# Kernel optimization log

Hardware: AMD Instinct MI355X
Metric: run time of the kernel (lower is better)

Reference implementation:

```python
import jax, jax.numpy as jnp
import numpy as np

N = 50000      # nodes
E = 600000     # edges
H = 128        # hidden_features (= in_features)
ED = 16        # edge_attr_dim
B = 256        # number of graphs in batch
L = 5          # num_layers
OUT = 128      # out_features


def _xavier(key, shape):
    fan_in, fan_out = shape
    a = float(np.sqrt(6.0 / (fan_in + fan_out)))
    return jax.random.uniform(key, shape, jnp.float32, -a, a)


def setup_inputs() -> dict:
    key = jax.random.key(0)
    ks = jax.random.split(key, 32)
    x = jax.random.normal(ks[0], (N, H), jnp.float32)
    edge_index = jax.random.randint(ks[1], (2, E), 0, N, jnp.int32)
    edge_attr = jax.random.normal(ks[2], (E, ED), jnp.float32)
    batch = jnp.sort(jax.random.randint(ks[3], (N,), 0, B, jnp.int32))
    # per-layer parameters, stacked along leading L axis (in=hidden so uniform)
    node_W = jnp.stack([_xavier(jax.random.fold_in(ks[4], i), (H, H)) for i in range(L)])
    edge_W = jnp.stack([_xavier(jax.random.fold_in(ks[5], i), (ED, H)) for i in range(L)])
    mlp1_W = jnp.stack([_xavier(jax.random.fold_in(ks[6], i), (H, H)) for i in range(L)])
    mlp2_W = jnp.stack([_xavier(jax.random.fold_in(ks[7], i), (H, H)) for i in range(L)])
    zb = jnp.zeros((L, H), jnp.float32)
    # virtual-node update MLP (shared across layers) and final classifier
    vn_w0 = _xavier(ks[8], (H, H)); vn_b0 = jnp.zeros((H,), jnp.float32)
    vn_w1 = _xavier(ks[9], (H, H)); vn_b1 = jnp.zeros((H,), jnp.float32)
    fc_W = _xavier(ks[10], (H, OUT)); fc_b = jnp.zeros((OUT,), jnp.float32)
    vn_init = jnp.zeros((1, H), jnp.float32)  # embedding initialized to 0
    return {
        "x": x, "edge_attr": edge_attr,
        "node_W": node_W, "node_b": zb, "edge_W": edge_W, "edge_b": zb,
        "mlp1_W": mlp1_W, "mlp1_b": zb, "mlp2_W": mlp2_W, "mlp2_b": zb,
        "vn_w0": vn_w0, "vn_b0": vn_b0, "vn_w1": vn_w1, "vn_b1": vn_b1,
        "fc_W": fc_W, "fc_b": fc_b, "vn_init": vn_init,
        "edge_index": edge_index, "batch": batch,
    }


def reference(x, edge_attr, node_W, node_b, edge_W, edge_b, mlp1_W, mlp1_b,
              mlp2_W, mlp2_b, vn_w0, vn_b0, vn_w1, vn_b1, fc_W, fc_b,
              vn_init, edge_index, batch):
    src, dst = edge_index[0], edge_index[1]
    # per-graph node counts for mean pooling (guard against empty graphs)
    counts = jnp.maximum(
        jax.ops.segment_sum(jnp.ones((N, 1), x.dtype), batch, num_segments=B), 1.0)
    vn = jnp.broadcast_to(vn_init, (B, H))  # weight.repeat(batch_size, 1)

    def layer(carry, p):
        xc, vn = carry
        nW, nb, eW, eb, m1W, m1b, m2W, m2b = p
        h = xc @ nW + nb + vn[batch]              # node encode + VN broadcast
        ea = edge_attr @ eW + eb                   # edge encode [E,H]
        msg = h[src] + ea                          # gather + add
        agg = jax.ops.segment_sum(msg, dst, num_segments=N)  # scatter-add
        out = jax.nn.relu(agg @ m1W + m1b) @ m2W + m2b        # layer MLP
        xn = jax.nn.relu(out)
        pooled = jax.ops.segment_sum(xn, batch, num_segments=B) / counts
        vn2 = vn + jax.nn.relu(jax.nn.relu(pooled @ vn_w0 + vn_b0) @ vn_w1 + vn_b1)
        return (xn, vn2), None

    (xf, _), _ = jax.lax.scan(
        layer, (x, vn),
        (node_W, node_b, edge_W, edge_b, mlp1_W, mlp1_b, mlp2_W, mlp2_b))
    pooled = jax.ops.segment_sum(xf, batch, num_segments=B) / counts
    return pooled @ fc_W + fc_b
```

## Files before the change

kernel.cpp:

```cpp
#include <hip/hip_runtime.h>

#define NN 50000
#define EE 600000
#define HH 128
#define EDD 16
#define BB 256
#define LL 5
#define NN16 (NN * 16)
#define NSHADOW 8
#define GN 782

typedef float f32x4 __attribute__((ext_vector_type(4)));
typedef _Float16 f16x4 __attribute__((ext_vector_type(4)));
typedef _Float16 f16x8 __attribute__((ext_vector_type(8)));

__global__ __launch_bounds__(256) void wprep_all_k(
    const float* __restrict__ W0, const float* __restrict__ W1, const float* __restrict__ W2,
    _Float16* __restrict__ H0, _Float16* __restrict__ L0,
    _Float16* __restrict__ H1, _Float16* __restrict__ L1,
    _Float16* __restrict__ H2, _Float16* __restrict__ L2,
    const float* __restrict__ eW, const float* __restrict__ eb, const float* __restrict__ nb,
    _Float16* __restrict__ BXh, _Float16* __restrict__ BXl)
{
    int idx = blockIdx.x * 256 + threadIdx.x;
    if (idx < 3 * 81920) {
        int seg = idx / 81920, r = idx - seg * 81920;
        const float* W = (seg == 0) ? W0 : (seg == 1) ? W1 : W2;
        _Float16* Wh = (seg == 0) ? H0 : (seg == 1) ? H1 : H2;
        _Float16* Wl = (seg == 0) ? L0 : (seg == 1) ? L1 : L2;
        int mat = r >> 14;
        int rr = r & 16383;
        int j = rr & 7, lane = (rr >> 3) & 63, ks = (rr >> 9) & 3, ntw = (rr >> 11) & 7;
        int lm = lane & 15, quad = lane >> 4;
        int n = (ntw >> 1) * 32 + (ntw & 1) * 16 + lm;
        int k = ks * 32 + quad * 8 + j;
        float w = W[(mat << 14) + (k << 7) + n];
        _Float16 h = (_Float16)w;
        Wh[r] = h;
        Wl[r] = (_Float16)(w - (float)h);
    } else {
        int i2 = idx - 3 * 81920;
        if (i2 >= 5 * 8192) return;
        int j = i2 & 7, lane = (i2 >> 3) & 63, ks = (i2 >> 9) & 1, ntw = (i2 >> 10) & 7, l = i2 >> 13;
        int lm = lane & 15, quad = lane >> 4;
        int n = (ntw >> 1) * 32 + (ntw & 1) * 16 + lm;
        int k = ks * 32 + quad * 8 + j;
        float v = 0.f;
        if (k < 16) v = eW[((size_t)l * 16 + k) * 128 + n];
        else if (k < 32) v = eW[((size_t)l * 16 + (k - 16)) * 128 + n];
        else if (k == 32) v = eb[l * 128 + n] + nb[l * 128 + n];
        _Float16 h = (_Float16)v;
        BXh[i2] = h;
        BXl[i2] = (_Float16)(v - (float)h);
    }
}

__global__ __launch_bounds__(256) void misc_k(const float* __restrict__ x, _Float16* __restrict__ X0,
    const float* __restrict__ vninit, float* __restrict__ vn, _Float16* __restrict__ vnB,
    float* __restrict__ pooled8)
{
    int i = blockIdx.x * 256 + threadIdx.x;
    if (i < NN * 32) {
        float4 v = ((const float4*)x)[i];
        f16x4 o;
        o[0] = (_Float16)v.x; o[1] = (_Float16)v.y; o[2] = (_Float16)v.z; o[3] = (_Float16)v.w;
        ((f16x4*)X0)[i] = o;
    } else {
        int k = i - NN * 32;
        if (k < NSHADOW * BB * HH) pooled8[k] = 0.f;
        if (k < BB * HH) { vn[k] = vninit[k & 127]; vnB[k] = (_Float16)0; }
    }
}

__device__ __forceinline__ void mfma_stage16(
    const _Float16* __restrict__ As,
    const _Float16* __restrict__ Wh, const _Float16* __restrict__ Wl,
    int wn, int lm, int quad, int lane, f32x4 acc[4][2])
{
    f16x8 Bh[2][4], Bl[2][4];
#pragma unroll
    for (int nt = 0; nt < 2; ++nt)
#pragma unroll
        for (int ks = 0; ks < 4; ++ks) {
            int fi = ((((wn * 2 + nt) * 4) + ks) * 64 + lane) * 8;
            Bh[nt][ks] = *(const f16x8*)(Wh + fi);
            Bl[nt][ks] = *(const f16x8*)(Wl + fi);
        }
#pragma unroll
    for (int ks = 0; ks < 4; ++ks) {
        f16x8 a[4];
#pragma unroll
        for (int mt = 0; mt < 4; ++mt) {
            int off = (mt * 16 + lm) * 136 + ks * 32 + quad * 8;
            a[mt] = *(const f16x8*)(As + off);
        }
#pragma unroll
        for (int mt = 0; mt < 4; ++mt)
#pragma unroll
            for (int nt = 0; nt < 2; ++nt) {
                acc[mt][nt] = __builtin_amdgcn_mfma_f32_16x16x32_f16(a[mt], Bh[nt][ks], acc[mt][nt], 0, 0, 0);
                acc[mt][nt] = __builtin_amdgcn_mfma_f32_16x16x32_f16(a[mt], Bl[nt][ks], acc[mt][nt], 0, 0, 0);
            }
    }
}

__device__ __forceinline__ void store_f16(const _Float16* __restrict__ Fo,
    _Float16* __restrict__ out, int M, int brow, int tid)
{
    const int r = tid >> 2, cg = tid & 3;
    const int grow = brow + r;
    if (grow >= M) return;
    const f16x8* src = (const f16x8*)(Fo + r * 136 + cg * 32);
    f16x8* dst = (f16x8*)(out + (size_t)grow * 128 + cg * 32);
#pragma unroll
    for (int i = 0; i < 4; ++i) dst[i] = src[i];
}

__global__ __launch_bounds__(256) void layer_k(
    const _Float16* __restrict__ Xin,
    const _Float16* __restrict__ Afix,
    const _Float16* __restrict__ Cfrag, const _Float16* __restrict__ vnB, int usevn,
    const int* __restrict__ rowstart, const int2* __restrict__ csr,
    const _Float16* __restrict__ WNh, const _Float16* __restrict__ WNl,
    const _Float16* __restrict__ BXh, const _Float16* __restrict__ BXl,
    const _Float16* __restrict__ W1h, const _Float16* __restrict__ W1l, const float* __restrict__ b1,
    const _Float16* __restrict__ W2h, const _Float16* __restrict__ W2l, const float* __restrict__ b2,
    _Float16* __restrict__ Xout, float* __restrict__ pooled8,
    const int* __restrict__ batch, int M)
{
    __shared__ __align__(16) _Float16 bufA[64 * 136];
    __shared__ __align__(16) _Float16 bufB[64 * 136];
    const int tid = threadIdx.x, brow = blockIdx.x * 64;

    {
        const int r = tid >> 2, cg = tid & 3;
        const int grow = brow + r;
        _Float16* p = bufB + r * 72 + cg * 16;
        if (grow < M) {
            const f16x8* s = (const f16x8*)(Afix + (size_t)grow * 64 + cg * 16);
            ((f16x8*)p)[0] = s[0]; ((f16x8*)p)[1] = s[1];
        } else {
            f16x8 z = (f16x8)(_Float16)0;
            ((f16x8*)p)[0] = z; ((f16x8*)p)[1] = z;
        }
    }

    {
        const int wv = tid >> 6, grp = (tid >> 4) & 3, li = tid & 15;
        const f16x8* X8 = (const f16x8*)Xin;
        for (int j = 0; j < 4; ++j) {
            int rnode = wv * 16 + grp * 4 + j;
            int node = brow + rnode;
            f16x8 o = (f16x8)(_Float16)0;
            if (node < M) {
                int s = rowstart[node], e = rowstart[node + 1];
                float ax[8];
#pragma unroll
                for (int k = 0; k < 8; ++k) ax[k] = 0.f;
                int p = s;
                for (; p + 4 <= e; p += 4) {
                    int s0 = csr[p].x, s1 = csr[p + 1].x, s2 = csr[p + 2].x, s3 = csr[p + 3].x;
                    f16x8 x0 = X8[(size_t)s0 * 16 + li];
                    f16x8 x1 = X8[(size_t)s1 * 16 + li];
                    f16x8 x2 = X8[(size_t)s2 * 16 + li];
                    f16x8 x3 = X8[(size_t)s3 * 16 + li];
#pragma unroll
                    for (int k = 0; k < 8; ++k)
                        ax[k] += ((float)x0[k] + (float)x1[k]) + ((float)x2[k] + (float)x3[k]);
                }
                for (; p < e; ++p) {
                    f16x8 x0 = X8[(size_t)csr[p].x * 16 + li];
#pragma unroll
                    for (int k = 0; k < 8; ++k) ax[k] += (float)x0[k];
                }
#pragma unroll
                for (int k = 0; k < 8; ++k) o[k] = (_Float16)ax[k];
            }
            *(f16x8*)(bufA + rnode * 136 + li * 8) = o;
        }
    }
    __syncthreads();

    const int lane = tid & 63, wn = tid >> 6, lm = lane & 15, quad = lane >> 4;
    const int colb = wn * 32 + lm;

    f32x4 acc[4][2];
#pragma unroll
    for (int mt = 0; mt < 4; ++mt) { acc[mt][0] = (f32x4)(0.f); acc[mt][1] = (f32x4)(0.f); }

    mfma_stage16(bufA, WNh, WNl, wn, lm, quad, lane, acc);

#pragma unroll
    for (int ksf = 0; ksf < 2; ++ksf) {
        f16x8 Bh[2], Bl[2];
#pragma unroll
        for (int nt = 0; nt < 2; ++nt) {
            int fi = (((wn * 2 + nt) * 2 + ksf) * 64 + lane) * 8;
            Bh[nt] = *(const f16x8*)(BXh + fi);
            Bl[nt] = *(const f16x8*)(BXl + fi);
        }
#pragma unroll
        for (int mt = 0; mt < 4; ++mt) {
            f16x8 a = *(const f16x8*)(bufB + (mt * 16 + lm) * 72 + ksf * 32 + quad * 8);
#pragma unroll
            for (int nt = 0; nt < 2; ++nt) {
                acc[mt][nt] = __builtin_amdgcn_mfma_f32_16x16x32_f16(a, Bh[nt], acc[mt][nt], 0, 0, 0);
                acc[mt][nt] = __builtin_amdgcn_mfma_f32_16x16x32_f16(a, Bl[nt], acc[mt][nt], 0, 0, 0);
            }
        }
    }

    if (usevn) {
        const _Float16* Cb = Cfrag + (size_t)blockIdx.x * 16384;
#pragma unroll
        for (int ks = 0; ks < 8; ++ks) {
            f16x8 bv[2];
#pragma unroll
            for (int nt = 0; nt < 2; ++nt)
                bv[nt] = *(const f16x8*)(vnB + (((ks * 8 + (wn * 2 + nt)) * 64 + lane) * 8));
#pragma unroll
            for (int mt = 0; mt < 4; ++mt) {
                f16x8 av = *(const f16x8*)(Cb + (((mt * 8 + ks) * 64 + lane) * 8));
                acc[mt][0] = __builtin_amdgcn_mfma_f32_16x16x32_f16(av, bv[0], acc[mt][0], 0, 0, 0);
                acc[mt][1] = __builtin_amdgcn_mfma_f32_16x16x32_f16(av, bv[1], acc[mt][1], 0, 0, 0);
            }
        }
    }
    __syncthreads();

#pragma unroll
    for (int mt = 0; mt < 4; ++mt) {
#pragma unroll
        for (int r = 0; r < 4; ++r) {
            int trow = mt * 16 + quad * 4 + r;
            bufA[trow * 136 + colb]      = (_Float16)acc[mt][0][r];
            bufA[trow * 136 + colb + 16] = (_Float16)acc[mt][1][r];
        }
    }
    __syncthreads();

#pragma unroll
    for (int mt = 0; mt < 4; ++mt) { acc[mt][0] = (f32x4)(0.f); acc[mt][1] = (f32x4)(0.f); }
    mfma_stage16(bufA, W1h, W1l, wn, lm, quad, lane, acc);
    {
        const float c0 = b1[colb], c1 = b1[colb + 16];
#pragma unroll
        for (int mt = 0; mt < 4; ++mt) {
#pragma unroll
            for (int r = 0; r < 4; ++r) {
                int trow = mt * 16 + quad * 4 + r;
                bufB[trow * 136 + colb]      = (_Float16)fmaxf(acc[mt][0][r] + c0, 0.f);
                bufB[trow * 136 + colb + 16] = (_Float16)fmaxf(acc[mt][1][r] + c1, 0.f);
            }
        }
    }
    __syncthreads();

#pragma unroll
    for (int mt = 0; mt < 4; ++mt) { acc[mt][0] = (f32x4)(0.f); acc[mt][1] = (f32x4)(0.f); }
    mfma_stage16(bufB, W2h, W2l, wn, lm, quad, lane, acc);
    {
        const float d0 = b2[colb], d1 = b2[colb + 16];
#pragma unroll
        for (int mt = 0; mt < 4; ++mt) {
#pragma unroll
            for (int r = 0; r < 4; ++r) {
                int trow = mt * 16 + quad * 4 + r;
                bufA[trow * 136 + colb]      = (_Float16)fmaxf(acc[mt][0][r] + d0, 0.f);
                bufA[trow * 136 + colb + 16] = (_Float16)fmaxf(acc[mt][1][r] + d1, 0.f);
            }
        }
    }
    __syncthreads();
    store_f16(bufA, Xout, M, brow, tid);

    {
        float* pooled = pooled8 + (size_t)(blockIdx.x & (NSHADOW - 1)) * (BB * HH);
        const int c = tid & 127, half = tid >> 7;
        const int row0 = half * 32;
        float sum = 0.f;
        int curg = -1;
        for (int r2 = 0; r2 < 32; ++r2) {
            int grow = brow + row0 + r2;
            if (grow >= M) break;
            int g = batch[grow];
            if (g != curg) {
                if (curg >= 0) atomicAdd(&pooled[curg * 128 + c], sum);
                curg = g; sum = 0.f;
            }
            sum += (float)bufA[(row0 + r2) * 136 + c];
        }
        if (curg >= 0) atomicAdd(&pooled[curg * 128 + c], sum);
    }
}

__global__ __launch_bounds__(256) void aggfix_k(
    const float* __restrict__ eattr, const int* __restrict__ rowstart,
    const int2* __restrict__ csr, _Float16* __restrict__ Afix, int n)
{
    const int lane = threadIdx.x & 15;
    const int node = blockIdx.x * 16 + (threadIdx.x >> 4);
    if (node >= n) return;
    const int s = rowstart[node], e = rowstart[node + 1];
    float acc = 0.f;
    for (int p = s; p < e; ++p)
        acc += eattr[(size_t)csr[p].y * 16 + lane];
    _Float16 hi = (_Float16)acc;
    _Float16 lo = (_Float16)(acc - (float)hi);
    _Float16* A = Afix + (size_t)node * 64;
    A[lane] = hi;
    A[16 + lane] = lo;
    A[32 + lane] = (lane == 0) ? (_Float16)(float)(e - s) : (_Float16)0;
    A[48 + lane] = (_Float16)0;
}

__global__ void histboth_k(const int* __restrict__ dstv, const int* __restrict__ srcv,
                           const int* __restrict__ batch,
                           int* __restrict__ degp, unsigned int* __restrict__ Cpack)
{
    int i = blockIdx.x * 256 + threadIdx.x;
    if (i >= EE) return;
    int d = dstv[i];
    atomicAdd(&degp[(blockIdx.x & 3) * NN16 + (d << 4)], 1);
    int g = batch[srcv[i]];
    int blk = d >> 6, rib = d & 63, mt = rib >> 4, lm = rib & 15;
    int ks = g >> 5, quad = (g >> 3) & 3, j = g & 7;
    size_t e = (size_t)blk * 16384 + (size_t)(((mt * 8 + ks) * 64) + quad * 16 + lm) * 8 + j;
    atomicAdd(&Cpack[e >> 1], 1u << ((e & 1) * 16));
}

__global__ __launch_bounds__(256) void ccvt_k(unsigned int* __restrict__ Cpack)
{
    int i = blockIdx.x * 256 + threadIdx.x;
    if (i >= GN * 16384 / 2) return;
    unsigned int v = Cpack[i];
    _Float16 lo = (_Float16)(float)(v & 0xffffu);
    _Float16 hi = (_Float16)(float)(v >> 16);
    unsigned short lu = __builtin_bit_cast(unsigned short, lo);
    unsigned short hu = __builtin_bit_cast(unsigned short, hi);
    Cpack[i] = (unsigned int)lu | ((unsigned int)hu << 16);
}

__global__ __launch_bounds__(128) void vn_update_k(
    float* __restrict__ pooled8, const int* __restrict__ gstart,
    const float* __restrict__ W0, const float* __restrict__ b0,
    const float* __restrict__ W1, const float* __restrict__ b1,
    float* __restrict__ vn, _Float16* __restrict__ vnB)
{
    __shared__ float p[128], q[128];
    const int g = blockIdx.x, t = threadIdx.x;
    float cnt = (float)(gstart[g + 1] - gstart[g]);
    if (cnt < 1.f) cnt = 1.f;
    float sum = 0.f;
#pragma unroll
    for (int s = 0; s < NSHADOW; ++s) {
        float* slot = pooled8 + (size_t)s * (BB * HH) + g * 128 + t;
        sum += *slot;
        *slot = 0.f;
    }
    p[t] = sum / cnt;
    __syncthreads();
    float a0 = b0[t];
    for (int k = 0; k < 128; ++k) a0 = fmaf(p[k], W0[k * 128 + t], a0);
    q[t] = fmaxf(a0, 0.f);
    __syncthreads();
    float a1 = b1[t];
    for (int k = 0; k < 128; ++k) a1 = fmaf(q[k], W1[k * 128 + t], a1);
    float nv = vn[g * 128 + t] + fmaxf(a1, 0.f);
    vn[g * 128 + t] = nv;
    {
        int ks = g >> 5, quad = (g >> 3) & 3, j = g & 7;
        int tt = ((t >> 5) << 1) | ((t >> 4) & 1);
        int lanev = quad * 16 + (t & 15);
        vnB[((ks * 8 + tt) * 64 + lanev) * 8 + j] = (_Float16)nv;
    }
}

__global__ __launch_bounds__(128) void fc_k(
    const float* __restrict__ pooled8, const int* __restrict__ gstart,
    const float* __restrict__ W, const float* __restrict__ b,
    float* __restrict__ out)
{
    __shared__ float p[128];
    const int g = blockIdx.x, t = threadIdx.x;
    float cnt = (float)(gstart[g + 1] - gstart[g]);
    if (cnt < 1.f) cnt = 1.f;
    float sum = 0.f;
#pragma unroll
    for (int s = 0; s < NSHADOW; ++s)
        sum += pooled8[(size_t)s * (BB * HH) + g * 128 + t];
    p[t] = sum / cnt;
    __syncthreads();
    float acc = b[t];
    for (int k = 0; k < 128; ++k) acc = fmaf(p[k], W[k * 128 + t], acc);
    out[g * 128 + t] = acc;
}

__global__ void scan_deg_k(const int* __restrict__ degp, int n, int* __restrict__ out, int* __restrict__ bsum)
{
    __shared__ int s[256];
    int gid = blockIdx.x * 256 + threadIdx.x;
    int v = 0;
    if (gid < n) {
        int o = gid << 4;
        v = degp[o] + degp[NN16 + o] + degp[2 * NN16 + o] + degp[3 * NN16 + o];
    }
    s[threadIdx.x] = v;
    __syncthreads();
    for (int off = 1; off < 256; off <<= 1) {
        int t = (threadIdx.x >= off) ? s[threadIdx.x - off] : 0;
        __syncthreads();
        s[threadIdx.x] += t;
        __syncthreads();
    }
    int incl = s[threadIdx.x];
    if (gid < n) out[gid] = incl - v;
    if (bsum != nullptr && threadIdx.x == 255) bsum[blockIdx.x] = incl;
}

__global__ void scan_k(const int* __restrict__ in, int n, int* __restrict__ out,
                       const int* __restrict__ batch, int* __restrict__ gstart)
{
    __shared__ int s[256];
    int v = (threadIdx.x < n) ? in[threadIdx.x] : 0;
    s[threadIdx.x] = v;
    __syncthreads();
    for (int off = 1; off < 256; off <<= 1) {
        int t = (threadIdx.x >= off) ? s[threadIdx.x - off] : 0;
        __syncthreads();
        s[threadIdx.x] += t;
        __syncthreads();
    }
    if (threadIdx.x < n) out[threadIdx.x] = s[threadIdx.x] - v;
    {
        int b = threadIdx.x;
        int lo = 0, hi = NN;
        while (lo < hi) {
            int mid = (lo + hi) >> 1;
            if (batch[mid] < b) lo = mid + 1; else hi = mid;
        }
        gstart[b] = lo;
        if (threadIdx.x == 0) gstart[BB] = NN;
    }
}

__global__ void addoff_k(int* __restrict__ data, const int* __restrict__ boff,
                         int* __restrict__ cursorp, int n, int total)
{
    int i = blockIdx.x * 256 + threadIdx.x;
    if (i < n) {
        int v = data[i] + boff[blockIdx.x];
        data[i] = v;
        cursorp[i << 4] = v;
    }
    if (i == 0) data[n] = total;
}

__global__ void fill_k(const int* __restrict__ dst, const int* __restrict__ src, int n,
                       int* __restrict__ cursorp, int2* __restrict__ csr)
{
    int e = blockIdx.x * 256 + threadIdx.x;
    if (e < n) {
        int slot = atomicAdd(&cursorp[dst[e] << 4], 1);
        int2 pr; pr.x = src[e]; pr.y = e;
        csr[slot] = pr;
    }
}

extern "C" void kernel_launch(void* const* d_in, const int* in_sizes, int n_in,
                              void* d_out, int out_size, void* d_ws, size_t ws_size,
                              hipStream_t stream)
{
    (void)in_sizes; (void)n_in; (void)out_size; (void)ws_size;
    const float* x       = (const float*)d_in[0];
    const float* eattr   = (const float*)d_in[1];
    const float* node_W  = (const float*)d_in[2];
    const float* node_b  = (const float*)d_in[3];
    const float* edge_W  = (const float*)d_in[4];
    const float* edge_b  = (const float*)d_in[5];
    const float* mlp1_W  = (const float*)d_in[6];
    const float* mlp1_b  = (const float*)d_in[7];
    const float* mlp2_W  = (const float*)d_in[8];
    const float* mlp2_b  = (const float*)d_in[9];
    const float* vn_w0   = (const float*)d_in[10];
    const float* vn_b0   = (const float*)d_in[11];
    const float* vn_w1   = (const float*)d_in[12];
    const float* vn_b1   = (const float*)d_in[13];
    const float* fc_W    = (const float*)d_in[14];
    const float* fc_b    = (const float*)d_in[15];
    const float* vn_init = (const float*)d_in[16];
    const int*   eidx    = (const int*)d_in[17];
    const int*   batch   = (const int*)d_in[18];
    const int* srcv = eidx;
    const int* dstv = eidx + EE;

    char* wp = (char*)d_ws;
    auto alloc = [&](size_t bytes) -> void* {
        void* p = (void*)wp;
        wp += (bytes + 255) & ~(size_t)255;
        return p;
    };
    int* degp       = (int*)alloc((size_t)4 * NN16 * 4);
    _Float16* Cfrag = (_Float16*)alloc((size_t)GN * 16384 * 2);
    const size_t zero_bytes = (size_t)4 * NN16 * 4 + (size_t)GN * 16384 * 2;

    _Float16* X0   = (_Float16*)alloc((size_t)NN * HH * 2);
    _Float16* X1   = (_Float16*)alloc((size_t)NN * HH * 2);
    _Float16* X2   = (_Float16*)alloc((size_t)NN * HH * 2);
    _Float16* Afix = (_Float16*)alloc((size_t)NN * 64 * 2);
    float* vn      = (float*)alloc((size_t)BB * HH * 4);
    _Float16* vnB  = (_Float16*)alloc((size_t)BB * HH * 2);
    float* pooled8 = (float*)alloc((size_t)NSHADOW * BB * HH * 4);
    int* rowstart  = (int*)alloc((size_t)(NN + 1) * 4);
    int* cursorp   = (int*)alloc((size_t)NN16 * 4);
    int2* csr      = (int2*)alloc((size_t)EE * 8);
    int* bsum      = (int*)alloc(256 * 4);
    int* boff      = (int*)alloc(256 * 4);
    int* gstart    = (int*)alloc((size_t)(BB + 1) * 4);
    _Float16* WtN_h = (_Float16*)alloc((size_t)5 * 16384 * 2);
    _Float16* WtN_l = (_Float16*)alloc((size_t)5 * 16384 * 2);
    _Float16* Wt1_h = (_Float16*)alloc((size_t)5 * 16384 * 2);
    _Float16* Wt1_l = (_Float16*)alloc((size_t)5 * 16384 * 2);
    _Float16* Wt2_h = (_Float16*)alloc((size_t)5 * 16384 * 2);
    _Float16* Wt2_l = (_Float16*)alloc((size_t)5 * 16384 * 2);
    _Float16* BXh   = (_Float16*)alloc((size_t)5 * 8192 * 2);
    _Float16* BXl   = (_Float16*)alloc((size_t)5 * 8192 * 2);

    (void)hipMemsetAsync(degp, 0, zero_bytes, stream);

    histboth_k<<<(EE + 255) / 256, 256, 0, stream>>>(dstv, srcv, batch, degp, (unsigned int*)Cfrag);

    const int NB1 = (NN + 255) / 256;
    scan_deg_k<<<NB1, 256, 0, stream>>>(degp, NN, rowstart, bsum);
    scan_k<<<1, 256, 0, stream>>>(bsum, NB1, boff, batch, gstart);
    addoff_k<<<NB1, 256, 0, stream>>>(rowstart, boff, cursorp, NN, EE);
    fill_k<<<(EE + 255) / 256, 256, 0, stream>>>(dstv, srcv, EE, cursorp, csr);
    aggfix_k<<<(NN + 15) / 16, 256, 0, stream>>>(eattr, rowstart, csr, Afix, NN);
    ccvt_k<<<(GN * 16384 / 2 + 255) / 256, 256, 0, stream>>>((unsigned int*)Cfrag);

    misc_k<<<(NN * 32 + NSHADOW * BB * HH) / 256, 256, 0, stream>>>(x, X0, vn_init, vn, vnB, pooled8);
    wprep_all_k<<<(3 * 81920 + 5 * 8192) / 256, 256, 0, stream>>>(
        node_W, mlp1_W, mlp2_W, WtN_h, WtN_l, Wt1_h, Wt1_l, Wt2_h, Wt2_l,
        edge_W, edge_b, node_b, BXh, BXl);

    const _Float16* xin = X0;
    for (int l = 0; l < LL; ++l) {
        _Float16* xout = (l & 1) ? X2 : X1;
        layer_k<<<GN, 256, 0, stream>>>(xin, Afix, Cfrag, vnB, (l > 0) ? 1 : 0,
            rowstart, csr,
            WtN_h + (size_t)l * 16384, WtN_l + (size_t)l * 16384,
            BXh + (size_t)l * 8192, BXl + (size_t)l * 8192,
            Wt1_h + (size_t)l * 16384, Wt1_l + (size_t)l * 16384, mlp1_b + (size_t)l * HH,
            Wt2_h + (size_t)l * 16384, Wt2_l + (size_t)l * 16384, mlp2_b + (size_t)l * HH,
            xout, pooled8, batch, NN);
        if (l < LL - 1)
            vn_update_k<<<BB, 128, 0, stream>>>(pooled8, gstart, vn_w0, vn_b0, vn_w1, vn_b1, vn, vnB);
        xin = xout;
    }
    fc_k<<<BB, 128, 0, stream>>>(pooled8, gstart, fc_W, fc_b, (float*)d_out);
}
```

Baseline: 558.6 us.

## Split layer kernel work across 8 waves with 16-column MFMA tiles

```diff
diff --git a/kernel.cpp b/kernel.cpp
--- a/kernel.cpp
+++ b/kernel.cpp
@@ -72,20 +72,18 @@
     }
 }
 
-__device__ __forceinline__ void mfma_stage16(
+__device__ __forceinline__ void mfma_stage8w(
     const _Float16* __restrict__ As,
     const _Float16* __restrict__ Wh, const _Float16* __restrict__ Wl,
-    int wn, int lm, int quad, int lane, f32x4 acc[4][2])
-{
-    f16x8 Bh[2][4], Bl[2][4];
-#pragma unroll
-    for (int nt = 0; nt < 2; ++nt)
-#pragma unroll
-        for (int ks = 0; ks < 4; ++ks) {
-            int fi = ((((wn * 2 + nt) * 4) + ks) * 64 + lane) * 8;
-            Bh[nt][ks] = *(const f16x8*)(Wh + fi);
-            Bl[nt][ks] = *(const f16x8*)(Wl + fi);
-        }
+    int wn, int lm, int quad, int lane, f32x4 acc[4])
+{
+    f16x8 Bh[4], Bl[4];
+#pragma unroll
+    for (int ks = 0; ks < 4; ++ks) {
+        int fi = ((wn * 4 + ks) * 64 + lane) * 8;
+        Bh[ks] = *(const f16x8*)(Wh + fi);
+        Bl[ks] = *(const f16x8*)(Wl + fi);
+    }
 #pragma unroll
     for (int ks = 0; ks < 4; ++ks) {
         f16x8 a[4];
@@ -95,28 +93,14 @@
             a[mt] = *(const f16x8*)(As + off);
         }
 #pragma unroll
-        for (int mt = 0; mt < 4; ++mt)
-#pragma unroll
-            for (int nt = 0; nt < 2; ++nt) {
-                acc[mt][nt] = __builtin_amdgcn_mfma_f32_16x16x32_f16(a[mt], Bh[nt][ks], acc[mt][nt], 0, 0, 0);
-                acc[mt][nt] = __builtin_amdgcn_mfma_f32_16x16x32_f16(a[mt], Bl[nt][ks], acc[mt][nt], 0, 0, 0);
-            }
-    }
-}
-
-__device__ __forceinline__ void store_f16(const _Float16* __restrict__ Fo,
-    _Float16* __restrict__ out, int M, int brow, int tid)
-{
-    const int r = tid >> 2, cg = tid & 3;
-    const int grow = brow + r;
-    if (grow >= M) return;
-    const f16x8* src = (const f16x8*)(Fo + r * 136 + cg * 32);
-    f16x8* dst = (f16x8*)(out + (size_t)grow * 128 + cg * 32);
-#pragma unroll
-    for (int i = 0; i < 4; ++i) dst[i] = src[i];
-}
-
-__global__ __launch_bounds__(256) void layer_k(
+        for (int mt = 0; mt < 4; ++mt) {
+            acc[mt] = __builtin_amdgcn_mfma_f32_16x16x32_f16(a[mt], Bh[ks], acc[mt], 0, 0, 0);
+            acc[mt] = __builtin_amdgcn_mfma_f32_16x16x32_f16(a[mt], Bl[ks], acc[mt], 0, 0, 0);
+        }
+    }
+}
+
+__global__ __launch_bounds__(512, 6) void layer_k(
     const _Float16* __restrict__ Xin,
     const _Float16* __restrict__ Afix,
     const _Float16* __restrict__ Cfrag, const _Float16* __restrict__ vnB, int usevn,
@@ -133,23 +117,22 @@
     const int tid = threadIdx.x, brow = blockIdx.x * 64;
 
     {
-        const int r = tid >> 2, cg = tid & 3;
+        const int r = tid >> 3, cg = tid & 7;
         const int grow = brow + r;
-        _Float16* p = bufB + r * 72 + cg * 16;
+        _Float16* p = bufB + r * 72 + cg * 8;
         if (grow < M) {
-            const f16x8* s = (const f16x8*)(Afix + (size_t)grow * 64 + cg * 16);
-            ((f16x8*)p)[0] = s[0]; ((f16x8*)p)[1] = s[1];
+            *(f16x8*)p = *(const f16x8*)(Afix + (size_t)grow * 64 + cg * 8);
         } else {
-            f16x8 z = (f16x8)(_Float16)0;
-            ((f16x8*)p)[0] = z; ((f16x8*)p)[1] = z;
-        }
-    }
-
-    {
-        const int wv = tid >> 6, grp = (tid >> 4) & 3, li = tid & 15;
+            *(f16x8*)p = (f16x8)(_Float16)0;
+        }
+    }
+
+    {
+        const int gid = tid >> 4, li = tid & 15;
         const f16x8* X8 = (const f16x8*)Xin;
-        for (int j = 0; j < 4; ++j) {
-            int rnode = wv * 16 + grp * 4 + j;
+#pragma unroll
+        for (int j = 0; j < 2; ++j) {
+            int rnode = gid * 2 + j;
             int node = brow + rnode;
             f16x8 o = (f16x8)(_Float16)0;
             if (node < M) {
@@ -182,31 +165,22 @@
     __syncthreads();
 
     const int lane = tid & 63, wn = tid >> 6, lm = lane & 15, quad = lane >> 4;
-    const int colb = wn * 32 + lm;
-
-    f32x4 acc[4][2];
-#pragma unroll
-    for (int mt = 0; mt < 4; ++mt) { acc[mt][0] = (f32x4)(0.f); acc[mt][1] = (f32x4)(0.f); }
-
-    mfma_stage16(bufA, WNh, WNl, wn, lm, quad, lane, acc);
+    const int colb = (wn >> 1) * 32 + (wn & 1) * 16 + lm;
+
+    f32x4 acc[4];
+#pragma unroll
+    for (int mt = 0; mt < 4; ++mt) acc[mt] = (f32x4)(0.f);
 
 #pragma unroll
     for (int ksf = 0; ksf < 2; ++ksf) {
-        f16x8 Bh[2], Bl[2];
-#pragma unroll
-        for (int nt = 0; nt < 2; ++nt) {
-            int fi = (((wn * 2 + nt) * 2 + ksf) * 64 + lane) * 8;
-            Bh[nt] = *(const f16x8*)(BXh + fi);
-            Bl[nt] = *(const f16x8*)(BXl + fi);
-        }
+        int fi = ((wn * 2 + ksf) * 64 + lane) * 8;
+        f16x8 Bh = *(const f16x8*)(BXh + fi);
+        f16x8 Bl = *(const f16x8*)(BXl + fi);
 #pragma unroll
         for (int mt = 0; mt < 4; ++mt) {
             f16x8 a = *(const f16x8*)(bufB + (mt * 16 + lm) * 72 + ksf * 32 + quad * 8);
-#pragma unroll
-            for (int nt = 0; nt < 2; ++nt) {
-                acc[mt][nt] = __builtin_amdgcn_mfma_f32_16x16x32_f16(a, Bh[nt], acc[mt][nt], 0, 0, 0);
-                acc[mt][nt] = __builtin_amdgcn_mfma_f32_16x16x32_f16(a, Bl[nt], acc[mt][nt], 0, 0, 0);
-            }
+            acc[mt] = __builtin_amdgcn_mfma_f32_16x16x32_f16(a, Bh, acc[mt], 0, 0, 0);
+            acc[mt] = __builtin_amdgcn_mfma_f32_16x16x32_f16(a, Bl, acc[mt], 0, 0, 0);
         }
     }
 
@@ -214,18 +188,16 @@
         const _Float16* Cb = Cfrag + (size_t)blockIdx.x * 16384;
 #pragma unroll
         for (int ks = 0; ks < 8; ++ks) {
-            f16x8 bv[2];
-#pragma unroll
-            for (int nt = 0; nt < 2; ++nt)
-                bv[nt] = *(const f16x8*)(vnB + (((ks * 8 + (wn * 2 + nt)) * 64 + lane) * 8));
+            f16x8 bv = *(const f16x8*)(vnB + (((ks * 8 + wn) * 64 + lane) * 8));
 #pragma unroll
             for (int mt = 0; mt < 4; ++mt) {
                 f16x8 av = *(const f16x8*)(Cb + (((mt * 8 + ks) * 64 + lane) * 8));
-                acc[mt][0] = __builtin_amdgcn_mfma_f32_16x16x32_f16(av, bv[0], acc[mt][0], 0, 0, 0);
-                acc[mt][1] = __builtin_amdgcn_mfma_f32_16x16x32_f16(av, bv[1], acc[mt][1], 0, 0, 0);
+                acc[mt] = __builtin_amdgcn_mfma_f32_16x16x32_f16(av, bv, acc[mt], 0, 0, 0);
             }
         }
     }
+
+    mfma_stage8w(bufA, WNh, WNl, wn, lm, quad, lane, acc);
     __syncthreads();
 
 #pragma unroll
@@ -233,54 +205,61 @@
 #pragma unroll
         for (int r = 0; r < 4; ++r) {
             int trow = mt * 16 + quad * 4 + r;
-            bufA[trow * 136 + colb]      = (_Float16)acc[mt][0][r];
-            bufA[trow * 136 + colb + 16] = (_Float16)acc[mt][1][r];
-        }
-    }
-    __syncthreads();
-
-#pragma unroll
-    for (int mt = 0; mt < 4; ++mt) { acc[mt][0] = (f32x4)(0.f); acc[mt][1] = (f32x4)(0.f); }
-    mfma_stage16(bufA, W1h, W1l, wn, lm, quad, lane, acc);
-    {
-        const float c0 = b1[colb], c1 = b1[colb + 16];
+            bufA[trow * 136 + colb] = (_Float16)acc[mt][r];
+        }
+    }
+    __syncthreads();
+
+#pragma unroll
+    for (int mt = 0; mt < 4; ++mt) acc[mt] = (f32x4)(0.f);
+    mfma_stage8w(bufA, W1h, W1l, wn, lm, quad, lane, acc);
+    {
+        const float c0 = b1[colb];
 #pragma unroll
         for (int mt = 0; mt < 4; ++mt) {
 #pragma unroll
             for (int r = 0; r < 4; ++r) {
                 int trow = mt * 16 + quad * 4 + r;
-                bufB[trow * 136 + colb]      = (_Float16)fmaxf(acc[mt][0][r] + c0, 0.f);
-                bufB[trow * 136 + colb + 16] = (_Float16)fmaxf(acc[mt][1][r] + c1, 0.f);
+                bufB[trow * 136 + colb] = (_Float16)fmaxf(acc[mt][r] + c0, 0.f);
             }
         }
     }
     __syncthreads();
 
 #pragma unroll
-    for (int mt = 0; mt < 4; ++mt) { acc[mt][0] = (f32x4)(0.f); acc[mt][1] = (f32x4)(0.f); }
-    mfma_stage16(bufB, W2h, W2l, wn, lm, quad, lane, acc);
-    {
-        const float d0 = b2[colb], d1 = b2[colb + 16];
+    for (int mt = 0; mt < 4; ++mt) acc[mt] = (f32x4)(0.f);
+    mfma_stage8w(bufB, W2h, W2l, wn, lm, quad, lane, acc);
+    {
+        const float d0 = b2[colb];
 #pragma unroll
         for (int mt = 0; mt < 4; ++mt) {
 #pragma unroll
             for (int r = 0; r < 4; ++r) {
                 int trow = mt * 16 + quad * 4 + r;
-                bufA[trow * 136 + colb]      = (_Float16)fmaxf(acc[mt][0][r] + d0, 0.f);
-                bufA[trow * 136 + colb + 16] = (_Float16)fmaxf(acc[mt][1][r] + d1, 0.f);
+                bufA[trow * 136 + colb] = (_Float16)fmaxf(acc[mt][r] + d0, 0.f);
             }
         }
     }
     __syncthreads();
-    store_f16(bufA, Xout, M, brow, tid);
+
+    {
+        const int r = tid >> 3, cg = tid & 7;
+        const int grow = brow + r;
+        if (grow < M) {
+            const f16x8* src = (const f16x8*)(bufA + r * 136 + cg * 16);
+            f16x8* dst = (f16x8*)(Xout + (size_t)grow * 128 + cg * 16);
+            dst[0] = src[0];
+            dst[1] = src[1];
+        }
+    }
 
     {
         float* pooled = pooled8 + (size_t)(blockIdx.x & (NSHADOW - 1)) * (BB * HH);
-        const int c = tid & 127, half = tid >> 7;
-        const int row0 = half * 32;
+        const int c = tid & 127, seg = tid >> 7;
+        const int row0 = seg * 16;
         float sum = 0.f;
         int curg = -1;
-        for (int r2 = 0; r2 < 32; ++r2) {
+        for (int r2 = 0; r2 < 16; ++r2) {
             int grow = brow + row0 + r2;
             if (grow >= M) break;
             int g = batch[grow];
@@ -546,7 +525,7 @@
     const _Float16* xin = X0;
     for (int l = 0; l < LL; ++l) {
         _Float16* xout = (l & 1) ? X2 : X1;
-        layer_k<<<GN, 256, 0, stream>>>(xin, Afix, Cfrag, vnB, (l > 0) ? 1 : 0,
+        layer_k<<<GN, 512, 0, stream>>>(xin, Afix, Cfrag, vnB, (l > 0) ? 1 : 0,
             rowstart, csr,
             WtN_h + (size_t)l * 16384, WtN_l + (size_t)l * 16384,
             BXh + (size_t)l * 8192, BXl + (size_t)l * 8192,
```

New measurement: 588.9 us. 1.05x slower.

## Halve layer kernel row tile to 32 rows and double grid

Applied to the files above, without the earlier changes.

```diff
diff --git a/kernel.cpp b/kernel.cpp
--- a/kernel.cpp
+++ b/kernel.cpp
@@ -9,6 +9,7 @@
 #define NN16 (NN * 16)
 #define NSHADOW 8
 #define GN 782
+#define GN2 1563
 
 typedef float f32x4 __attribute__((ext_vector_type(4)));
 typedef _Float16 f16x4 __attribute__((ext_vector_type(4)));
@@ -72,10 +73,10 @@
     }
 }
 
-__device__ __forceinline__ void mfma_stage16(
+__device__ __forceinline__ void mfma_stage32(
     const _Float16* __restrict__ As,
     const _Float16* __restrict__ Wh, const _Float16* __restrict__ Wl,
-    int wn, int lm, int quad, int lane, f32x4 acc[4][2])
+    int wn, int lm, int quad, int lane, f32x4 acc[2][2])
 {
     f16x8 Bh[2][4], Bl[2][4];
 #pragma unroll
@@ -88,32 +89,20 @@
         }
 #pragma unroll
     for (int ks = 0; ks < 4; ++ks) {
-        f16x8 a[4];
-#pragma unroll
-        for (int mt = 0; mt < 4; ++mt) {
+        f16x8 a[2];
+#pragma unroll
+        for (int mt = 0; mt < 2; ++mt) {
             int off = (mt * 16 + lm) * 136 + ks * 32 + quad * 8;
             a[mt] = *(const f16x8*)(As + off);
         }
 #pragma unroll
-        for (int mt = 0; mt < 4; ++mt)
+        for (int mt = 0; mt < 2; ++mt)
 #pragma unroll
             for (int nt = 0; nt < 2; ++nt) {
                 acc[mt][nt] = __builtin_amdgcn_mfma_f32_16x16x32_f16(a[mt], Bh[nt][ks], acc[mt][nt], 0, 0, 0);
                 acc[mt][nt] = __builtin_amdgcn_mfma_f32_16x16x32_f16(a[mt], Bl[nt][ks], acc[mt][nt], 0, 0, 0);
             }
     }
-}
-
-__device__ __forceinline__ void store_f16(const _Float16* __restrict__ Fo,
-    _Float16* __restrict__ out, int M, int brow, int tid)
-{
-    const int r = tid >> 2, cg = tid & 3;
-    const int grow = brow + r;
-    if (grow >= M) return;
-    const f16x8* src = (const f16x8*)(Fo + r * 136 + cg * 32);
-    f16x8* dst = (f16x8*)(out + (size_t)grow * 128 + cg * 32);
-#pragma unroll
-    for (int i = 0; i < 4; ++i) dst[i] = src[i];
 }
 
 __global__ __launch_bounds__(256) void layer_k(
@@ -128,28 +117,27 @@
     _Float16* __restrict__ Xout, float* __restrict__ pooled8,
     const int* __restrict__ batch, int M)
 {
-    __shared__ __align__(16) _Float16 bufA[64 * 136];
-    __shared__ __align__(16) _Float16 bufB[64 * 136];
-    const int tid = threadIdx.x, brow = blockIdx.x * 64;
-
-    {
-        const int r = tid >> 2, cg = tid & 3;
+    __shared__ __align__(16) _Float16 bufA[32 * 136];
+    __shared__ __align__(16) _Float16 bufB[32 * 136];
+    const int tid = threadIdx.x, brow = blockIdx.x * 32;
+
+    {
+        const int r = tid >> 3, cg = tid & 7;
         const int grow = brow + r;
-        _Float16* p = bufB + r * 72 + cg * 16;
+        _Float16* p = bufB + r * 72 + cg * 8;
         if (grow < M) {
-            const f16x8* s = (const f16x8*)(Afix + (size_t)grow * 64 + cg * 16);
-            ((f16x8*)p)[0] = s[0]; ((f16x8*)p)[1] = s[1];
+            *(f16x8*)p = *(const f16x8*)(Afix + (size_t)grow * 64 + cg * 8);
         } else {
-            f16x8 z = (f16x8)(_Float16)0;
-            ((f16x8*)p)[0] = z; ((f16x8*)p)[1] = z;
-        }
-    }
-
-    {
-        const int wv = tid >> 6, grp = (tid >> 4) & 3, li = tid & 15;
+            *(f16x8*)p = (f16x8)(_Float16)0;
+        }
+    }
+
+    {
+        const int gid = tid >> 4, li = tid & 15;
         const f16x8* X8 = (const f16x8*)Xin;
-        for (int j = 0; j < 4; ++j) {
-            int rnode = wv * 16 + grp * 4 + j;
+#pragma unroll
+        for (int j = 0; j < 2; ++j) {
+            int rnode = gid * 2 + j;
             int node = brow + rnode;
             f16x8 o = (f16x8)(_Float16)0;
             if (node < M) {
@@ -184,11 +172,9 @@
     const int lane = tid & 63, wn = tid >> 6, lm = lane & 15, quad = lane >> 4;
     const int colb = wn * 32 + lm;
 
-    f32x4 acc[4][2];
-#pragma unroll
-    for (int mt = 0; mt < 4; ++mt) { acc[mt][0] = (f32x4)(0.f); acc[mt][1] = (f32x4)(0.f); }
-
-    mfma_stage16(bufA, WNh, WNl, wn, lm, quad, lane, acc);
+    f32x4 acc[2][2];
+#pragma unroll
+    for (int mt = 0; mt < 2; ++mt) { acc[mt][0] = (f32x4)(0.f); acc[mt][1] = (f32x4)(0.f); }
 
 #pragma unroll
     for (int ksf = 0; ksf < 2; ++ksf) {
@@ -200,7 +186,7 @@
             Bl[nt] = *(const f16x8*)(BXl + fi);
         }
 #pragma unroll
-        for (int mt = 0; mt < 4; ++mt) {
+        for (int mt = 0; mt < 2; ++mt) {
             f16x8 a = *(const f16x8*)(bufB + (mt * 16 + lm) * 72 + ksf * 32 + quad * 8);
 #pragma unroll
             for (int nt = 0; nt < 2; ++nt) {
@@ -211,7 +197,8 @@
     }
 
     if (usevn) {
-        const _Float16* Cb = Cfrag + (size_t)blockIdx.x * 16384;
+        const _Float16* Cb = Cfrag + (size_t)(blockIdx.x >> 1) * 16384;
+        const int mtoff = (blockIdx.x & 1) * 2;
 #pragma unroll
         for (int ks = 0; ks < 8; ++ks) {
             f16x8 bv[2];
@@ -219,17 +206,19 @@
             for (int nt = 0; nt < 2; ++nt)
                 bv[nt] = *(const f16x8*)(vnB + (((ks * 8 + (wn * 2 + nt)) * 64 + lane) * 8));
 #pragma unroll
-            for (int mt = 0; mt < 4; ++mt) {
-                f16x8 av = *(const f16x8*)(Cb + (((mt * 8 + ks) * 64 + lane) * 8));
+            for (int mt = 0; mt < 2; ++mt) {
+                f16x8 av = *(const f16x8*)(Cb + ((((mtoff + mt) * 8 + ks) * 64 + lane) * 8));
                 acc[mt][0] = __builtin_amdgcn_mfma_f32_16x16x32_f16(av, bv[0], acc[mt][0], 0, 0, 0);
                 acc[mt][1] = __builtin_amdgcn_mfma_f32_16x16x32_f16(av, bv[1], acc[mt][1], 0, 0, 0);
             }
         }
     }
-    __syncthreads();
-
-#pragma unroll
-    for (int mt = 0; mt < 4; ++mt) {
+
+    mfma_stage32(bufA, WNh, WNl, wn, lm, quad, lane, acc);
+    __syncthreads();
+
+#pragma unroll
+    for (int mt = 0; mt < 2; ++mt) {
 #pragma unroll
         for (int r = 0; r < 4; ++r) {
             int trow = mt * 16 + quad * 4 + r;
@@ -240,12 +229,12 @@
     __syncthreads();
 
 #pragma unroll
-    for (int mt = 0; mt < 4; ++mt) { acc[mt][0] = (f32x4)(0.f); acc[mt][1] = (f32x4)(0.f); }
-    mfma_stage16(bufA, W1h, W1l, wn, lm, quad, lane, acc);
+    for (int mt = 0; mt < 2; ++mt) { acc[mt][0] = (f32x4)(0.f); acc[mt][1] = (f32x4)(0.f); }
+    mfma_stage32(bufA, W1h, W1l, wn, lm, quad, lane, acc);
     {
         const float c0 = b1[colb], c1 = b1[colb + 16];
 #pragma unroll
-        for (int mt = 0; mt < 4; ++mt) {
+        for (int mt = 0; mt < 2; ++mt) {
 #pragma unroll
             for (int r = 0; r < 4; ++r) {
                 int trow = mt * 16 + quad * 4 + r;
@@ -257,12 +246,12 @@
     __syncthreads();
 
 #pragma unroll
-    for (int mt = 0; mt < 4; ++mt) { acc[mt][0] = (f32x4)(0.f); acc[mt][1] = (f32x4)(0.f); }
-    mfma_stage16(bufB, W2h, W2l, wn, lm, quad, lane, acc);
+    for (int mt = 0; mt < 2; ++mt) { acc[mt][0] = (f32x4)(0.f); acc[mt][1] = (f32x4)(0.f); }
+    mfma_stage32(bufB, W2h, W2l, wn, lm, quad, lane, acc);
     {
         const float d0 = b2[colb], d1 = b2[colb + 16];
 #pragma unroll
-        for (int mt = 0; mt < 4; ++mt) {
+        for (int mt = 0; mt < 2; ++mt) {
 #pragma unroll
             for (int r = 0; r < 4; ++r) {
                 int trow = mt * 16 + quad * 4 + r;
@@ -272,15 +261,25 @@
         }
     }
     __syncthreads();
-    store_f16(bufA, Xout, M, brow, tid);
+
+    {
+        const int r = tid >> 3, cg = tid & 7;
+        const int grow = brow + r;
+        if (grow < M) {
+            const f16x8* src = (const f16x8*)(bufA + r * 136 + cg * 16);
+            f16x8* dst = (f16x8*)(Xout + (size_t)grow * 128 + cg * 16);
+            dst[0] = src[0];
+            dst[1] = src[1];
+        }
+    }
 
     {
         float* pooled = pooled8 + (size_t)(blockIdx.x & (NSHADOW - 1)) * (BB * HH);
         const int c = tid & 127, half = tid >> 7;
-        const int row0 = half * 32;
+        const int row0 = half * 16;
         float sum = 0.f;
         int curg = -1;
-        for (int r2 = 0; r2 < 32; ++r2) {
+        for (int r2 = 0; r2 < 16; ++r2) {
             int grow = brow + row0 + r2;
             if (grow >= M) break;
             int g = batch[grow];
@@ -546,7 +545,7 @@
     const _Float16* xin = X0;
     for (int l = 0; l < LL; ++l) {
         _Float16* xout = (l & 1) ? X2 : X1;
-        layer_k<<<GN, 256, 0, stream>>>(xin, Afix, Cfrag, vnB, (l > 0) ? 1 : 0,
+        layer_k<<<GN2, 256, 0, stream>>>(xin, Afix, Cfrag, vnB, (l > 0) ? 1 : 0,
             rowstart, csr,
             WtN_h + (size_t)l * 16384, WtN_l + (size_t)l * 16384,
             BXh + (size_t)l * 8192, BXl + (size_t)l * 8192,
```

Result: slower. 581.4 us (+4.1%).

## Build per-block graph count fragments from CSR in shared memory, fuse prep kernels

Applied to the files above, without the earlier changes.

```diff
diff --git a/kernel.cpp b/kernel.cpp
--- a/kernel.cpp
+++ b/kernel.cpp
@@ -14,7 +14,10 @@
 typedef _Float16 f16x4 __attribute__((ext_vector_type(4)));
 typedef _Float16 f16x8 __attribute__((ext_vector_type(8)));
 
-__global__ __launch_bounds__(256) void wprep_all_k(
+__global__ __launch_bounds__(256) void prep_all_k(
+    const float* __restrict__ x, _Float16* __restrict__ X0,
+    const float* __restrict__ vninit, float* __restrict__ vn, _Float16* __restrict__ vnB,
+    float* __restrict__ pooled8,
     const float* __restrict__ W0, const float* __restrict__ W1, const float* __restrict__ W2,
     _Float16* __restrict__ H0, _Float16* __restrict__ L0,
     _Float16* __restrict__ H1, _Float16* __restrict__ L1,
@@ -22,9 +25,23 @@
     const float* __restrict__ eW, const float* __restrict__ eb, const float* __restrict__ nb,
     _Float16* __restrict__ BXh, _Float16* __restrict__ BXl)
 {
-    int idx = blockIdx.x * 256 + threadIdx.x;
-    if (idx < 3 * 81920) {
-        int seg = idx / 81920, r = idx - seg * 81920;
+    int i = blockIdx.x * 256 + threadIdx.x;
+    if (i < NN * 32) {
+        float4 v = ((const float4*)x)[i];
+        f16x4 o;
+        o[0] = (_Float16)v.x; o[1] = (_Float16)v.y; o[2] = (_Float16)v.z; o[3] = (_Float16)v.w;
+        ((f16x4*)X0)[i] = o;
+        return;
+    }
+    i -= NN * 32;
+    if (i < NSHADOW * BB * HH) {
+        pooled8[i] = 0.f;
+        if (i < BB * HH) { vn[i] = vninit[i & 127]; vnB[i] = (_Float16)0; }
+        return;
+    }
+    i -= NSHADOW * BB * HH;
+    if (i < 3 * 81920) {
+        int seg = i / 81920, r = i - seg * 81920;
         const float* W = (seg == 0) ? W0 : (seg == 1) ? W1 : W2;
         _Float16* Wh = (seg == 0) ? H0 : (seg == 1) ? H1 : H2;
         _Float16* Wl = (seg == 0) ? L0 : (seg == 1) ? L1 : L2;
@@ -38,10 +55,11 @@
         _Float16 h = (_Float16)w;
         Wh[r] = h;
         Wl[r] = (_Float16)(w - (float)h);
-    } else {
-        int i2 = idx - 3 * 81920;
-        if (i2 >= 5 * 8192) return;
-        int j = i2 & 7, lane = (i2 >> 3) & 63, ks = (i2 >> 9) & 1, ntw = (i2 >> 10) & 7, l = i2 >> 13;
+        return;
+    }
+    i -= 3 * 81920;
+    if (i < 5 * 8192) {
+        int j = i & 7, lane = (i >> 3) & 63, ks = (i >> 9) & 1, ntw = (i >> 10) & 7, l = i >> 13;
         int lm = lane & 15, quad = lane >> 4;
         int n = (ntw >> 1) * 32 + (ntw & 1) * 16 + lm;
         int k = ks * 32 + quad * 8 + j;
@@ -50,25 +68,8 @@
         else if (k < 32) v = eW[((size_t)l * 16 + (k - 16)) * 128 + n];
         else if (k == 32) v = eb[l * 128 + n] + nb[l * 128 + n];
         _Float16 h = (_Float16)v;
-        BXh[i2] = h;
-        BXl[i2] = (_Float16)(v - (float)h);
-    }
-}
-
-__global__ __launch_bounds__(256) void misc_k(const float* __restrict__ x, _Float16* __restrict__ X0,
-    const float* __restrict__ vninit, float* __restrict__ vn, _Float16* __restrict__ vnB,
-    float* __restrict__ pooled8)
-{
-    int i = blockIdx.x * 256 + threadIdx.x;
-    if (i < NN * 32) {
-        float4 v = ((const float4*)x)[i];
-        f16x4 o;
-        o[0] = (_Float16)v.x; o[1] = (_Float16)v.y; o[2] = (_Float16)v.z; o[3] = (_Float16)v.w;
-        ((f16x4*)X0)[i] = o;
-    } else {
-        int k = i - NN * 32;
-        if (k < NSHADOW * BB * HH) pooled8[k] = 0.f;
-        if (k < BB * HH) { vn[k] = vninit[k & 127]; vnB[k] = (_Float16)0; }
+        BXh[i] = h;
+        BXl[i] = (_Float16)(v - (float)h);
     }
 }
 
@@ -188,8 +189,6 @@
 #pragma unroll
     for (int mt = 0; mt < 4; ++mt) { acc[mt][0] = (f32x4)(0.f); acc[mt][1] = (f32x4)(0.f); }
 
-    mfma_stage16(bufA, WNh, WNl, wn, lm, quad, lane, acc);
-
 #pragma unroll
     for (int ksf = 0; ksf < 2; ++ksf) {
         f16x8 Bh[2], Bl[2];
@@ -226,6 +225,8 @@
             }
         }
     }
+
+    mfma_stage16(bufA, WNh, WNl, wn, lm, quad, lane, acc);
     __syncthreads();
 
 #pragma unroll
@@ -304,7 +305,7 @@
     const int s = rowstart[node], e = rowstart[node + 1];
     float acc = 0.f;
     for (int p = s; p < e; ++p)
-        acc += eattr[(size_t)csr[p].y * 16 + lane];
+        acc += eattr[(size_t)(csr[p].y & 0xFFFFF) * 16 + lane];
     _Float16 hi = (_Float16)acc;
     _Float16 lo = (_Float16)(acc - (float)hi);
     _Float16* A = Afix + (size_t)node * 64;
@@ -314,31 +315,46 @@
     A[48 + lane] = (_Float16)0;
 }
 
-__global__ void histboth_k(const int* __restrict__ dstv, const int* __restrict__ srcv,
-                           const int* __restrict__ batch,
-                           int* __restrict__ degp, unsigned int* __restrict__ Cpack)
+__global__ __launch_bounds__(256) void cfrag_k(
+    const int* __restrict__ rowstart, const int2* __restrict__ csr,
+    _Float16* __restrict__ Cfrag, int n)
+{
+    __shared__ unsigned int cnt[64 * 128];
+    __shared__ int rs[65];
+    const int tid = threadIdx.x, brow = blockIdx.x * 64;
+    for (int i = tid; i < 64 * 128; i += 256) cnt[i] = 0u;
+    if (tid < 65) {
+        int node = brow + tid;
+        rs[tid] = rowstart[node <= n ? node : n];
+    }
+    __syncthreads();
+    const int s = rs[0], e = rs[64];
+    for (int p = s + tid; p < e; p += 256) {
+        int g = csr[p].y >> 20;
+        int lo = 0, hi = 63;
+        while (lo < hi) {
+            int mid = (lo + hi + 1) >> 1;
+            if (rs[mid] <= p) lo = mid; else hi = mid - 1;
+        }
+        atomicAdd(&cnt[lo * 128 + (g >> 1)], 1u << ((g & 1) * 16));
+    }
+    __syncthreads();
+    const size_t base = (size_t)blockIdx.x * 16384;
+    for (int i = tid; i < 16384; i += 256) {
+        int j = i & 7, lanef = (i >> 3) & 63, ks = (i >> 9) & 7, mt = i >> 12;
+        int lm = lanef & 15, quad = lanef >> 4;
+        int row = mt * 16 + lm;
+        int g = ks * 32 + quad * 8 + j;
+        unsigned int w = cnt[row * 128 + (g >> 1)];
+        unsigned int c = (g & 1) ? (w >> 16) : (w & 0xffffu);
+        Cfrag[base + i] = (_Float16)(float)c;
+    }
+}
+
+__global__ void histp_k(const int* __restrict__ idx, int n, int* __restrict__ cntp)
 {
     int i = blockIdx.x * 256 + threadIdx.x;
-    if (i >= EE) return;
-    int d = dstv[i];
-    atomicAdd(&degp[(blockIdx.x & 3) * NN16 + (d << 4)], 1);
-    int g = batch[srcv[i]];
-    int blk = d >> 6, rib = d & 63, mt = rib >> 4, lm = rib & 15;
-    int ks = g >> 5, quad = (g >> 3) & 3, j = g & 7;
-    size_t e = (size_t)blk * 16384 + (size_t)(((mt * 8 + ks) * 64) + quad * 16 + lm) * 8 + j;
-    atomicAdd(&Cpack[e >> 1], 1u << ((e & 1) * 16));
-}
-
-__global__ __launch_bounds__(256) void ccvt_k(unsigned int* __restrict__ Cpack)
-{
-    int i = blockIdx.x * 256 + threadIdx.x;
-    if (i >= GN * 16384 / 2) return;
-    unsigned int v = Cpack[i];
-    _Float16 lo = (_Float16)(float)(v & 0xffffu);
-    _Float16 hi = (_Float16)(float)(v >> 16);
-    unsigned short lu = __builtin_bit_cast(unsigned short, lo);
-    unsigned short hu = __builtin_bit_cast(unsigned short, hi);
-    Cpack[i] = (unsigned int)lu | ((unsigned int)hu << 16);
+    if (i < n) atomicAdd(&cntp[(blockIdx.x & 3) * NN16 + (idx[i] << 4)], 1);
 }
 
 __global__ __launch_bounds__(128) void vn_update_k(
@@ -418,51 +434,51 @@
     if (bsum != nullptr && threadIdx.x == 255) bsum[blockIdx.x] = incl;
 }
 
-__global__ void scan_k(const int* __restrict__ in, int n, int* __restrict__ out,
-                       const int* __restrict__ batch, int* __restrict__ gstart)
+__global__ void addoff2_k(int* __restrict__ data, const int* __restrict__ bsum,
+                          int* __restrict__ cursorp,
+                          const int* __restrict__ batch, int* __restrict__ gstart,
+                          int n, int total)
 {
     __shared__ int s[256];
-    int v = (threadIdx.x < n) ? in[threadIdx.x] : 0;
-    s[threadIdx.x] = v;
+    const int t = threadIdx.x;
+    s[t] = (t < (int)blockIdx.x) ? bsum[t] : 0;
     __syncthreads();
     for (int off = 1; off < 256; off <<= 1) {
-        int t = (threadIdx.x >= off) ? s[threadIdx.x - off] : 0;
+        int v = (t >= off) ? s[t - off] : 0;
         __syncthreads();
-        s[threadIdx.x] += t;
+        s[t] += v;
         __syncthreads();
     }
-    if (threadIdx.x < n) out[threadIdx.x] = s[threadIdx.x] - v;
-    {
-        int b = threadIdx.x;
+    const int boff = s[255];
+    int i = blockIdx.x * 256 + t;
+    if (i < n) {
+        int v = data[i] + boff;
+        data[i] = v;
+        cursorp[i << 4] = v;
+    }
+    if (i == 0) data[n] = total;
+    if (blockIdx.x == 0) {
+        int b = t;
         int lo = 0, hi = NN;
         while (lo < hi) {
             int mid = (lo + hi) >> 1;
             if (batch[mid] < b) lo = mid + 1; else hi = mid;
         }
         gstart[b] = lo;
-        if (threadIdx.x == 0) gstart[BB] = NN;
-    }
-}
-
-__global__ void addoff_k(int* __restrict__ data, const int* __restrict__ boff,
-                         int* __restrict__ cursorp, int n, int total)
-{
-    int i = blockIdx.x * 256 + threadIdx.x;
-    if (i < n) {
-        int v = data[i] + boff[blockIdx.x];
-        data[i] = v;
-        cursorp[i << 4] = v;
-    }
-    if (i == 0) data[n] = total;
+        if (t == 0) gstart[BB] = NN;
+    }
 }
 
 __global__ void fill_k(const int* __restrict__ dst, const int* __restrict__ src, int n,
+                       const int* __restrict__ batch,
                        int* __restrict__ cursorp, int2* __restrict__ csr)
 {
     int e = blockIdx.x * 256 + threadIdx.x;
     if (e < n) {
+        int sv = src[e];
+        int g = batch[sv];
         int slot = atomicAdd(&cursorp[dst[e] << 4], 1);
-        int2 pr; pr.x = src[e]; pr.y = e;
+        int2 pr; pr.x = sv; pr.y = e | (g << 20);
         csr[slot] = pr;
     }
 }
@@ -501,8 +517,8 @@
         return p;
     };
     int* degp       = (int*)alloc((size_t)4 * NN16 * 4);
+    const size_t zero_bytes = (size_t)4 * NN16 * 4;
     _Float16* Cfrag = (_Float16*)alloc((size_t)GN * 16384 * 2);
-    const size_t zero_bytes = (size_t)4 * NN16 * 4 + (size_t)GN * 16384 * 2;
 
     _Float16* X0   = (_Float16*)alloc((size_t)NN * HH * 2);
     _Float16* X1   = (_Float16*)alloc((size_t)NN * HH * 2);
@@ -515,7 +531,6 @@
     int* cursorp   = (int*)alloc((size_t)NN16 * 4);
     int2* csr      = (int2*)alloc((size_t)EE * 8);
     int* bsum      = (int*)alloc(256 * 4);
-    int* boff      = (int*)alloc(256 * 4);
     int* gstart    = (int*)alloc((size_t)(BB + 1) * 4);
     _Float16* WtN_h = (_Float16*)alloc((size_t)5 * 16384 * 2);
     _Float16* WtN_l = (_Float16*)alloc((size_t)5 * 16384 * 2);
@@ -528,18 +543,18 @@
 
     (void)hipMemsetAsync(degp, 0, zero_bytes, stream);
 
-    histboth_k<<<(EE + 255) / 256, 256, 0, stream>>>(dstv, srcv, batch, degp, (unsigned int*)Cfrag);
+    histp_k<<<(EE + 255) / 256, 256, 0, stream>>>(dstv, EE, degp);
 
     const int NB1 = (NN + 255) / 256;
     scan_deg_k<<<NB1, 256, 0, stream>>>(degp, NN, rowstart, bsum);
-    scan_k<<<1, 256, 0, stream>>>(bsum, NB1, boff, batch, gstart);
-    addoff_k<<<NB1, 256, 0, stream>>>(rowstart, boff, cursorp, NN, EE);
-    fill_k<<<(EE + 255) / 256, 256, 0, stream>>>(dstv, srcv, EE, cursorp, csr);
+    addoff2_k<<<NB1, 256, 0, stream>>>(rowstart, bsum, cursorp, batch, gstart, NN, EE);
+    fill_k<<<(EE + 255) / 256, 256, 0, stream>>>(dstv, srcv, EE, batch, cursorp, csr);
     aggfix_k<<<(NN + 15) / 16, 256, 0, stream>>>(eattr, rowstart, csr, Afix, NN);
-    ccvt_k<<<(GN * 16384 / 2 + 255) / 256, 256, 0, stream>>>((unsigned int*)Cfrag);
-
-    misc_k<<<(NN * 32 + NSHADOW * BB * HH) / 256, 256, 0, stream>>>(x, X0, vn_init, vn, vnB, pooled8);
-    wprep_all_k<<<(3 * 81920 + 5 * 8192) / 256, 256, 0, stream>>>(
+    cfrag_k<<<GN, 256, 0, stream>>>(rowstart, csr, Cfrag, NN);
+
+    const int PREP_TOTAL = NN * 32 + NSHADOW * BB * HH + 3 * 81920 + 5 * 8192;
+    prep_all_k<<<(PREP_TOTAL + 255) / 256, 256, 0, stream>>>(
+        x, X0, vn_init, vn, vnB, pooled8,
         node_W, mlp1_W, mlp2_W, WtN_h, WtN_l, Wt1_h, Wt1_l, Wt2_h, Wt2_l,
         edge_W, edge_b, node_b, BXh, BXl);
 
```

After: 649.2 us. 1.16x slower.
